# Performance work log

Hardware: AMD Instinct MI355X
Metric: run time of the kernel (lower is better)

## Reference

```python
import jax, jax.numpy as jnp
import numpy as np

B, T = 64, 4096
H, I, F = 256, 7, 5
# MLP pyramid: in=H+F=261 -> 2^8..2^3 -> itera_dim
DIMS = [H + F, 256, 128, 64, 32, 16, 8, I]


def _uniform(key, shape, fan_in):
    s = 1.0 / np.sqrt(fan_in)
    return jax.random.uniform(key, shape, jnp.float32, -s, s)


def setup_inputs() -> dict:
    key = jax.random.key(0)
    ks = jax.random.split(key, 32)
    inp = {"x": jax.random.normal(ks[0], (B, T, I + F), jnp.float32)}
    # RNN params (torch nn.RNN layout: W_ih [H,I], W_hh [H,H])
    inp["W_ih"] = _uniform(ks[1], (H, I), H)
    inp["W_hh"] = _uniform(ks[2], (H, H), H)
    inp["b_ih"] = _uniform(ks[3], (H,), H)
    inp["b_hh"] = _uniform(ks[4], (H,), H)
    # fc_V linears
    for j, (din, dout) in enumerate(zip(DIMS[:-1], DIMS[1:])):
        inp[f"W{j}"] = _uniform(ks[5 + 2 * j], (dout, din), din)
        inp[f"b{j}"] = _uniform(ks[6 + 2 * j], (dout,), din)
    return inp


def reference(x, W_ih, W_hh, b_ih, b_hh,
              W0, b0, W1, b1, W2, b2, W3, b3, W4, b4, W5, b5, W6, b6):
    x_itera = x[..., :I]          # [B,T,I]
    x_fixed = x[..., I:]          # [B,T,F]
    # precompute input projection for the whole sequence (one big GEMM)
    xW = jnp.einsum('bti,hi->bth', x_itera, W_ih) + b_ih + b_hh  # [B,T,H]

    def step(h, xw_t):
        h = jnp.tanh(xw_t + h @ W_hh.T)
        return h, h

    h0 = jnp.zeros((x.shape[0], H), x.dtype)
    h_last, ht = jax.lax.scan(step, h0, jnp.swapaxes(xW, 0, 1))  # ht: [T,B,H]
    ht = jnp.swapaxes(ht, 0, 1)                                  # [B,T,H]

    z = jnp.concatenate([ht, x_fixed], axis=-1)                  # [B,T,H+F]
    for W, b in ((W0, b0), (W1, b1), (W2, b2), (W3, b3), (W4, b4), (W5, b5)):
        z = jax.nn.leaky_relu(z @ W.T + b, 0.01)
    ot = z @ W6.T + b6                                           # [B,T,I]
    return ot, h_last[None]                                      # ht_last: [1,B,H]
```

## Files before the change

### kernel.cpp

```cpp
#include <hip/hip_runtime.h>

#define BB 64
#define TT 4096
#define HH 256
#define NTOK (BB * TT)

typedef _Float16 f16;
typedef _Float16 f16x2 __attribute__((ext_vector_type(2)));
typedef _Float16 f16x8 __attribute__((ext_vector_type(8)));
typedef float f32x4 __attribute__((ext_vector_type(4)));
typedef unsigned int uint;
typedef unsigned short ushort;
typedef uint uint4v __attribute__((ext_vector_type(4)));

__device__ __forceinline__ uint packf16(float a, float b) {
    ushort lo = __builtin_bit_cast(ushort, (f16)a);
    ushort hi = __builtin_bit_cast(ushort, (f16)b);
    return (uint)lo | ((uint)hi << 16);
}

__global__ __launch_bounds__(256) void rnn_wswz_kernel(const float* __restrict__ Whh,
                                                       uint4v* __restrict__ Wsw) {
    int gid = blockIdx.x * 256 + threadIdx.x;
    if (gid >= 8192) return;
    int tid = gid >> 5, fi = gid & 31;
    int mt = fi >> 3, ks = fi & 7;
    int lane = tid & 63, w = tid >> 6;
    int hd = w * 64 + mt * 16 + (lane & 15);
    int kb = ks * 32 + ((lane >> 4) << 3);
    const float* p = Whh + hd * 256 + kb;
    uint4v v;
    v.x = packf16(p[0], p[1]);
    v.y = packf16(p[2], p[3]);
    v.z = packf16(p[4], p[5]);
    v.w = packf16(p[6], p[7]);
    Wsw[gid] = v;
}

__global__ __launch_bounds__(256) void bfrag_prep_kernel(const float* __restrict__ W,
                                                         uint4v* __restrict__ dst,
                                                         int N, int Kreal, int KS, int NT) {
    int gid = blockIdx.x * 256 + threadIdx.x;
    if (gid >= NT * KS * 64) return;
    int lane = gid & 63;
    int t = gid >> 6;
    int ks = t % KS, nt = t / KS;
    int n = nt * 16 + (lane & 15);
    int kb = ks * 32 + (lane >> 4) * 8;
    float f[8];
#pragma unroll
    for (int j = 0; j < 8; ++j) {
        int k = kb + j;
        f[j] = (n < N && k < Kreal) ? W[n * Kreal + k] : 0.f;
    }
    uint4v v;
    v.x = packf16(f[0], f[1]);
    v.y = packf16(f[2], f[3]);
    v.z = packf16(f[4], f[5]);
    v.w = packf16(f[6], f[7]);
    dst[gid] = v;
}

__global__ __launch_bounds__(256) __attribute__((amdgpu_waves_per_eu(1, 1))) void rnn_kernel(
        const float* __restrict__ x, const uint4v* __restrict__ Wsw,
        const float* __restrict__ Wih, const float* __restrict__ bih,
        const float* __restrict__ bhh, f16* __restrict__ ht, float* __restrict__ hlast) {
    const int b = blockIdx.x, tid = threadIdx.x;
    const int lane = tid & 63, w = tid >> 6;
    const int q = lane >> 4, bl = lane & 15;
    const int d = w * 64 + ((bl >> 2) << 4) + (q << 2) + (bl & 3);
    __shared__ __align__(16) f16 hbuf[2][256];
    __shared__ uint4 xs[2][128];

    uint4v wv[32];
    {
        const uint4v* wp = Wsw + (size_t)tid * 32;
#pragma unroll
        for (int i = 0; i < 32; ++i) wv[i] = wp[i];
    }
#pragma unroll
    for (int i = 0; i < 32; ++i) asm volatile("" : "+v"(wv[i]));

    float wih[7];
#pragma unroll
    for (int i = 0; i < 7; ++i) wih[i] = Wih[d * 7 + i];
    const float bias = bih[d] + bhh[d];

    const float* xb = x + (size_t)b * TT * 12;
    uint4 xpre = make_uint4(0, 0, 0, 0);
    if (tid < 128) {
        int row = tid >> 1, u = tid & 1;
        xs[0][row * 2 + u] = *(const uint4*)(xb + row * 12 + u * 4);
        xpre = *(const uint4*)(xb + (64 + row) * 12 + u * 4);
        ((uint*)hbuf[0])[tid] = 0;
    }
    __syncthreads();

    f16* htp = ht + (size_t)b * TT * 256 + d;

    for (int tb = 0; tb < 256; ++tb) {
#pragma unroll
        for (int k = 0; k < 16; ++k) {
            const int t = tb * 16 + k;
            const int cur = k & 1;
            const int tile = (t >> 6) & 1, tstep = t & 63;

            const float4 xa = ((const float4*)xs[tile])[tstep * 2];
            const float4 xc = ((const float4*)xs[tile])[tstep * 2 + 1];
            float xw = fmaf(xa.x, wih[0], bias);
            xw = fmaf(xa.y, wih[1], xw);
            xw = fmaf(xa.z, wih[2], xw);
            xw = fmaf(xa.w, wih[3], xw);
            xw = fmaf(xc.x, wih[4], xw);
            xw = fmaf(xc.y, wih[5], xw);
            xw = fmaf(xc.z, wih[6], xw);

            const uint4v* hq = (const uint4v*)hbuf[cur];
            uint4v hfr[8];
#pragma unroll
            for (int ks = 0; ks < 8; ++ks) hfr[ks] = hq[ks * 4 + q];

            f32x4 acc[4];
#pragma unroll
            for (int mt = 0; mt < 4; ++mt) acc[mt] = (f32x4){0.f, 0.f, 0.f, 0.f};
#pragma unroll
            for (int ks = 0; ks < 8; ++ks) {
                f16x8 hb = __builtin_bit_cast(f16x8, hfr[ks]);
#pragma unroll
                for (int mt = 0; mt < 4; ++mt)
                    acc[mt] = __builtin_amdgcn_mfma_f32_16x16x32_f16(
                        __builtin_bit_cast(f16x8, wv[mt * 8 + ks]), hb, acc[mt], 0, 0, 0);
            }

            float t0[4];
#pragma unroll
            for (int mt = 0; mt < 4; ++mt) {
                float a01 = (bl & 1) ? acc[mt][1] : acc[mt][0];
                float a23 = (bl & 1) ? acc[mt][3] : acc[mt][2];
                t0[mt] = (bl & 2) ? a23 : a01;
            }
            float u0 = (bl & 4) ? t0[1] : t0[0];
            float u1 = (bl & 4) ? t0[3] : t0[2];
            float pre = ((bl & 8) ? u1 : u0) + xw;

            float e = __expf(-2.0f * pre);
            float rr = __builtin_amdgcn_rcpf(1.0f + e);
            float h = fmaf(2.0f, rr, -1.0f);

            f16 hf = (f16)h;
            hbuf[cur ^ 1][d] = hf;
            htp[(size_t)t * 256] = hf;
            if (tb == 255 && k == 15) hlast[b * 256 + d] = h;

            if (tstep == 32 && tid < 128) {
                int row = tid >> 1, u = tid & 1;
                xs[tile ^ 1][row * 2 + u] = xpre;
                int nt = (t & ~63) + 128 + row;
                if (nt > TT - 1) nt = TT - 1;
                xpre = *(const uint4*)(xb + nt * 12 + u * 4);
            }
            asm volatile("s_waitcnt lgkmcnt(0)\n\ts_barrier" ::: "memory");
        }
    }
}

struct MlpB {
    const uint4v* bf[7];
    const float* bias[7];
};

template <int KS, int NT, bool MSPLIT>
__device__ __forceinline__ void mfma_layer(const uint4v* __restrict__ Bf,
                                           const float* __restrict__ bias, int Nreal,
                                           const uint4v* zin, uint4v* zout,
                                           int w, int lane, int m15, int q) {
    constexpr int NW = MSPLIT ? NT : (NT / 4);
    constexpr int MW = MSPLIT ? 1 : 4;
    const int ntb = MSPLIT ? 0 : w * NW;
    const int mtb = MSPLIT ? w : 0;
    f32x4 acc[MW][NW];
#pragma unroll
    for (int i = 0; i < MW; ++i)
#pragma unroll
        for (int j = 0; j < NW; ++j) acc[i][j] = (f32x4){0.f, 0.f, 0.f, 0.f};

#pragma unroll
    for (int ks = 0; ks < KS; ++ks) {
        f16x8 a[MW];
#pragma unroll
        for (int mt = 0; mt < MW; ++mt)
            a[mt] = __builtin_bit_cast(f16x8, zin[((mtb + mt) * 16 + m15) * 37 + ks * 4 + q]);
#pragma unroll
        for (int nt = 0; nt < NW; ++nt) {
            f16x8 b = __builtin_bit_cast(f16x8, Bf[((size_t)(ntb + nt) * KS + ks) * 64 + lane]);
#pragma unroll
            for (int mt = 0; mt < MW; ++mt)
                acc[mt][nt] =
                    __builtin_amdgcn_mfma_f32_16x16x32_f16(a[mt], b, acc[mt][nt], 0, 0, 0);
        }
    }
    f16* zo = (f16*)zout;
#pragma unroll
    for (int nt = 0; nt < NW; ++nt) {
        const int col = (ntb + nt) * 16 + m15;
        const float bv = (col < Nreal) ? bias[col] : 0.f;
#pragma unroll
        for (int mt = 0; mt < MW; ++mt) {
#pragma unroll
            for (int r = 0; r < 4; ++r) {
                float v = acc[mt][nt][r] + bv;
                v = fmaxf(v, 0.01f * v);
                const int row = (mtb + mt) * 16 + q * 4 + r;
                zo[row * 296 + col] = (f16)v;
            }
        }
    }
}

__global__ __launch_bounds__(256) void mlp_kernel(const f16* __restrict__ ht,
                                                  const float* __restrict__ x,
                                                  MlpB P, float* __restrict__ out) {
    __shared__ uint4v z0[64 * 37];
    __shared__ uint4v z1[64 * 37];
    const int tid = threadIdx.x;
    const int w = tid >> 6, lane = tid & 63;
    const int m15 = lane & 15, q = lane >> 4;
    const int tok0 = blockIdx.x * 64;

    for (int i = tid; i < 64 * 32; i += 256) {
        int r = i >> 5, u = i & 31;
        z0[r * 37 + u] = ((const uint4v*)(ht + (size_t)(tok0 + r) * 256))[u];
    }
    for (int i = tid; i < 64 * 5; i += 256) {
        int r = i / 5, u = 32 + (i % 5);
        uint4v v = {0u, 0u, 0u, 0u};
        if (u == 32) {
            const float* xp = x + (size_t)(tok0 + r) * 12 + 7;
            v.x = packf16(xp[0], xp[1]);
            v.y = packf16(xp[2], xp[3]);
            v.z = packf16(xp[4], 0.f);
        }
        z0[r * 37 + u] = v;
    }
    __syncthreads();

    mfma_layer<9, 16, false>(P.bf[0], P.bias[0], 256, z0, z1, w, lane, m15, q);
    __syncthreads();
    mfma_layer<8, 8, false>(P.bf[1], P.bias[1], 128, z1, z0, w, lane, m15, q);
    __syncthreads();
    mfma_layer<4, 4, false>(P.bf[2], P.bias[2], 64, z0, z1, w, lane, m15, q);
    __syncthreads();
    mfma_layer<2, 2, true>(P.bf[3], P.bias[3], 32, z1, z0, w, lane, m15, q);
    __syncthreads();
    mfma_layer<1, 1, true>(P.bf[4], P.bias[4], 16, z0, z1, w, lane, m15, q);
    __syncthreads();
    mfma_layer<1, 1, true>(P.bf[5], P.bias[5], 8, z1, z0, w, lane, m15, q);
    __syncthreads();

    {
        f16x8 a = __builtin_bit_cast(f16x8, z0[(w * 16 + m15) * 37 + q]);
        f16x8 b = __builtin_bit_cast(f16x8, P.bf[6][lane]);
        f32x4 acc = (f32x4){0.f, 0.f, 0.f, 0.f};
        acc = __builtin_amdgcn_mfma_f32_16x16x32_f16(a, b, acc, 0, 0, 0);
        if (m15 < 7) {
            const float bv = P.bias[6][m15];
#pragma unroll
            for (int r = 0; r < 4; ++r)
                out[(size_t)(tok0 + w * 16 + q * 4 + r) * 7 + m15] = acc[r] + bv;
        }
    }
}

extern "C" void kernel_launch(void* const* d_in, const int* in_sizes, int n_in,
                              void* d_out, int out_size, void* d_ws, size_t ws_size,
                              hipStream_t stream) {
    const float* x = (const float*)d_in[0];
    const float* Wih = (const float*)d_in[1];
    const float* Whh = (const float*)d_in[2];
    const float* bih = (const float*)d_in[3];
    const float* bhh = (const float*)d_in[4];
    const float* W[7];
    const float* bb[7];
    for (int j = 0; j < 7; ++j) {
        W[j] = (const float*)d_in[5 + 2 * j];
        bb[j] = (const float*)d_in[6 + 2 * j];
    }
    float* out = (float*)d_out;

    static const int Kd[7] = {261, 256, 128, 64, 32, 16, 8};
    static const int Nd[7] = {256, 128, 64, 32, 16, 8, 7};
    static const int KSd[7] = {9, 8, 4, 2, 1, 1, 1};
    static const int NTd[7] = {16, 8, 4, 2, 1, 1, 1};

    char* ws = (char*)d_ws;
    f16* ht = (f16*)ws;
    size_t off = (size_t)NTOK * HH * 2;
    uint4v* Wsw = (uint4v*)(ws + off);
    off += (size_t)8192 * 16;
    uint4v* bfp[7];
    for (int j = 0; j < 7; ++j) {
        bfp[j] = (uint4v*)(ws + off);
        off += (size_t)NTd[j] * KSd[j] * 64 * 16;
    }

    rnn_wswz_kernel<<<32, 256, 0, stream>>>(Whh, Wsw);
    for (int j = 0; j < 7; ++j) {
        int cnt = NTd[j] * KSd[j] * 64;
        bfrag_prep_kernel<<<(cnt + 255) / 256, 256, 0, stream>>>(W[j], bfp[j], Nd[j], Kd[j],
                                                                 KSd[j], NTd[j]);
    }

    rnn_kernel<<<BB, 256, 0, stream>>>(x, Wsw, Wih, bih, bhh, ht, out + (size_t)NTOK * 7);

    MlpB P;
    for (int j = 0; j < 7; ++j) {
        P.bf[j] = bfp[j];
        P.bias[j] = bb[j];
    }
    mlp_kernel<<<NTOK / 64, 256, 0, stream>>>(ht, x, P, out);
}
```

Before: 2.112 ms.

## Split RNN recurrence across 8 waves with K-split MFMA and batched ht stores

The recurrent kernel now uses 512 threads (8 waves) per batch row. Each wave owns 32 hidden units instead of 64, so it holds half as many W_hh fragments and issues half as many MFMAs per step. The K dimension is split into two independent accumulator chains that are summed afterwards, which shortens the serial MFMA dependency per timestep. Global ht writes are buffered in registers and flushed every 16 steps, and tanh switches to exp2. The aim is to cut per-step latency in the sequential recurrence, at the cost of a wider barrier across 8 waves and some duplicated lanes that are masked off as non-writers.

```diff
diff --git a/kernel.cpp b/kernel.cpp
--- a/kernel.cpp
+++ b/kernel.cpp
@@ -23,10 +23,10 @@
                                                        uint4v* __restrict__ Wsw) {
     int gid = blockIdx.x * 256 + threadIdx.x;
     if (gid >= 8192) return;
-    int tid = gid >> 5, fi = gid & 31;
+    int tid = gid >> 4, fi = gid & 15;
     int mt = fi >> 3, ks = fi & 7;
     int lane = tid & 63, w = tid >> 6;
-    int hd = w * 64 + mt * 16 + (lane & 15);
+    int hd = w * 32 + mt * 16 + (lane & 15);
     int kb = ks * 32 + ((lane >> 4) << 3);
     const float* p = Whh + hd * 256 + kb;
     uint4v v;
@@ -61,25 +61,26 @@
     dst[gid] = v;
 }
 
-__global__ __launch_bounds__(256) __attribute__((amdgpu_waves_per_eu(1, 1))) void rnn_kernel(
+__global__ __launch_bounds__(512) __attribute__((amdgpu_waves_per_eu(2, 2))) void rnn_kernel(
         const float* __restrict__ x, const uint4v* __restrict__ Wsw,
         const float* __restrict__ Wih, const float* __restrict__ bih,
         const float* __restrict__ bhh, f16* __restrict__ ht, float* __restrict__ hlast) {
     const int b = blockIdx.x, tid = threadIdx.x;
     const int lane = tid & 63, w = tid >> 6;
     const int q = lane >> 4, bl = lane & 15;
-    const int d = w * 64 + ((bl >> 2) << 4) + (q << 2) + (bl & 3);
+    const int d = w * 32 + ((bl >> 3) << 4) + (q << 2) + (bl & 3);
+    const bool writer = (bl & 4) == 0;
     __shared__ __align__(16) f16 hbuf[2][256];
     __shared__ uint4 xs[2][128];
 
-    uint4v wv[32];
+    uint4v wv[16];
     {
-        const uint4v* wp = Wsw + (size_t)tid * 32;
-#pragma unroll
-        for (int i = 0; i < 32; ++i) wv[i] = wp[i];
-    }
-#pragma unroll
-    for (int i = 0; i < 32; ++i) asm volatile("" : "+v"(wv[i]));
+        const uint4v* wp = Wsw + (size_t)tid * 16;
+#pragma unroll
+        for (int i = 0; i < 16; ++i) wv[i] = wp[i];
+    }
+#pragma unroll
+    for (int i = 0; i < 16; ++i) asm volatile("" : "+v"(wv[i]));
 
     float wih[7];
 #pragma unroll
@@ -97,6 +98,7 @@
     __syncthreads();
 
     f16* htp = ht + (size_t)b * TT * 256 + d;
+    ushort hst[16];
 
     for (int tb = 0; tb < 256; ++tb) {
 #pragma unroll
@@ -104,6 +106,26 @@
             const int t = tb * 16 + k;
             const int cur = k & 1;
             const int tile = (t >> 6) & 1, tstep = t & 63;
+
+            const uint4v* hq = (const uint4v*)hbuf[cur];
+            uint4v hfr[8];
+#pragma unroll
+            for (int ks = 0; ks < 8; ++ks) hfr[ks] = hq[ks * 4 + q];
+
+            f32x4 a0 = (f32x4){0.f, 0.f, 0.f, 0.f}, a1 = a0, a2 = a0, a3 = a0;
+#pragma unroll
+            for (int kk = 0; kk < 4; ++kk) {
+                f16x8 hlo = __builtin_bit_cast(f16x8, hfr[kk]);
+                f16x8 hhi = __builtin_bit_cast(f16x8, hfr[4 + kk]);
+                a0 = __builtin_amdgcn_mfma_f32_16x16x32_f16(
+                    __builtin_bit_cast(f16x8, wv[kk]), hlo, a0, 0, 0, 0);
+                a1 = __builtin_amdgcn_mfma_f32_16x16x32_f16(
+                    __builtin_bit_cast(f16x8, wv[4 + kk]), hhi, a1, 0, 0, 0);
+                a2 = __builtin_amdgcn_mfma_f32_16x16x32_f16(
+                    __builtin_bit_cast(f16x8, wv[8 + kk]), hlo, a2, 0, 0, 0);
+                a3 = __builtin_amdgcn_mfma_f32_16x16x32_f16(
+                    __builtin_bit_cast(f16x8, wv[12 + kk]), hhi, a3, 0, 0, 0);
+            }
 
             const float4 xa = ((const float4*)xs[tile])[tstep * 2];
             const float4 xc = ((const float4*)xs[tile])[tstep * 2 + 1];
@@ -115,42 +137,25 @@
             xw = fmaf(xc.y, wih[5], xw);
             xw = fmaf(xc.z, wih[6], xw);
 
-            const uint4v* hq = (const uint4v*)hbuf[cur];
-            uint4v hfr[8];
-#pragma unroll
-            for (int ks = 0; ks < 8; ++ks) hfr[ks] = hq[ks * 4 + q];
-
-            f32x4 acc[4];
-#pragma unroll
-            for (int mt = 0; mt < 4; ++mt) acc[mt] = (f32x4){0.f, 0.f, 0.f, 0.f};
-#pragma unroll
-            for (int ks = 0; ks < 8; ++ks) {
-                f16x8 hb = __builtin_bit_cast(f16x8, hfr[ks]);
-#pragma unroll
-                for (int mt = 0; mt < 4; ++mt)
-                    acc[mt] = __builtin_amdgcn_mfma_f32_16x16x32_f16(
-                        __builtin_bit_cast(f16x8, wv[mt * 8 + ks]), hb, acc[mt], 0, 0, 0);
-            }
-
-            float t0[4];
-#pragma unroll
-            for (int mt = 0; mt < 4; ++mt) {
-                float a01 = (bl & 1) ? acc[mt][1] : acc[mt][0];
-                float a23 = (bl & 1) ? acc[mt][3] : acc[mt][2];
-                t0[mt] = (bl & 2) ? a23 : a01;
-            }
-            float u0 = (bl & 4) ? t0[1] : t0[0];
-            float u1 = (bl & 4) ? t0[3] : t0[2];
-            float pre = ((bl & 8) ? u1 : u0) + xw;
-
-            float e = __expf(-2.0f * pre);
+            f32x4 acc0 = a0 + a1;
+            f32x4 acc1 = a2 + a3;
+
+            float s0 = (bl & 8) ? acc1[0] : acc0[0];
+            float s1 = (bl & 8) ? acc1[1] : acc0[1];
+            float s2 = (bl & 8) ? acc1[2] : acc0[2];
+            float s3 = (bl & 8) ? acc1[3] : acc0[3];
+            float p01 = (bl & 1) ? s1 : s0;
+            float p23 = (bl & 1) ? s3 : s2;
+            float pre = ((bl & 2) ? p23 : p01) + xw;
+
+            float e = __builtin_amdgcn_exp2f(-2.885390082f * pre);
             float rr = __builtin_amdgcn_rcpf(1.0f + e);
             float h = fmaf(2.0f, rr, -1.0f);
 
             f16 hf = (f16)h;
-            hbuf[cur ^ 1][d] = hf;
-            htp[(size_t)t * 256] = hf;
-            if (tb == 255 && k == 15) hlast[b * 256 + d] = h;
+            if (writer) hbuf[cur ^ 1][d] = hf;
+            hst[k] = __builtin_bit_cast(ushort, hf);
+            if (tb == 255 && k == 15 && writer) hlast[b * 256 + d] = h;
 
             if (tstep == 32 && tid < 128) {
                 int row = tid >> 1, u = tid & 1;
@@ -160,6 +165,12 @@
                 xpre = *(const uint4*)(xb + nt * 12 + u * 4);
             }
             asm volatile("s_waitcnt lgkmcnt(0)\n\ts_barrier" ::: "memory");
+        }
+        if (writer) {
+            const size_t base = (size_t)(tb * 16) * 256;
+#pragma unroll
+            for (int k = 0; k < 16; ++k)
+                htp[base + (size_t)k * 256] = __builtin_bit_cast(f16, hst[k]);
         }
     }
 }
@@ -310,7 +321,7 @@
                                                                  KSd[j], NTd[j]);
     }
 
-    rnn_kernel<<<BB, 256, 0, stream>>>(x, Wsw, Wih, bih, bhh, ht, out + (size_t)NTOK * 7);
+    rnn_kernel<<<BB, 512, 0, stream>>>(x, Wsw, Wih, bih, bhh, ht, out + (size_t)NTOK * 7);
 
     MlpB P;
     for (int j = 0; j < 7; ++j) {
```

Result: faster. 1.900 ms (-10.0%).

## Pack two batch sequences per RNN block and batch h_t global stores

Applied to the files above, without the earlier changes.

The RNN kernel now runs two independent batch sequences per 512-thread block (32 blocks instead of 64), each group of four waves holding its own copy of the W_hh fragments and its own shared hbuf/xs. The MFMA recurrence is moved ahead of the input projection so the latency-critical matmul starts first, and tanh uses a raw exp2 intrinsic. h_t values are buffered in registers for 16 steps and written to global memory after each block of steps, taking stores out of the per-step critical path. The shared barrier now couples two sequences, and running two waves per EU halves the per-wave register budget, which may cause register pressure or spills.

```diff
diff --git a/kernel.cpp b/kernel.cpp
--- a/kernel.cpp
+++ b/kernel.cpp
@@ -25,8 +25,8 @@
     if (gid >= 8192) return;
     int tid = gid >> 5, fi = gid & 31;
     int mt = fi >> 3, ks = fi & 7;
-    int lane = tid & 63, w = tid >> 6;
-    int hd = w * 64 + mt * 16 + (lane & 15);
+    int lane = tid & 63, wb = tid >> 6;
+    int hd = wb * 64 + mt * 16 + (lane & 15);
     int kb = ks * 32 + ((lane >> 4) << 3);
     const float* p = Whh + hd * 256 + kb;
     uint4v v;
@@ -61,20 +61,23 @@
     dst[gid] = v;
 }
 
-__global__ __launch_bounds__(256) __attribute__((amdgpu_waves_per_eu(1, 1))) void rnn_kernel(
+__global__ __launch_bounds__(512) __attribute__((amdgpu_waves_per_eu(2, 2))) void rnn_kernel(
         const float* __restrict__ x, const uint4v* __restrict__ Wsw,
         const float* __restrict__ Wih, const float* __restrict__ bih,
         const float* __restrict__ bhh, f16* __restrict__ ht, float* __restrict__ hlast) {
-    const int b = blockIdx.x, tid = threadIdx.x;
+    const int tid = threadIdx.x;
     const int lane = tid & 63, w = tid >> 6;
+    const int wb = w & 3, bat = w >> 2;
+    const int b = blockIdx.x * 2 + bat;
+    const int gtid = tid & 255;
     const int q = lane >> 4, bl = lane & 15;
-    const int d = w * 64 + ((bl >> 2) << 4) + (q << 2) + (bl & 3);
-    __shared__ __align__(16) f16 hbuf[2][256];
-    __shared__ uint4 xs[2][128];
+    const int d = wb * 64 + ((bl >> 2) << 4) + (q << 2) + (bl & 3);
+    __shared__ __align__(16) f16 hbuf[2][2][256];
+    __shared__ uint4 xs[2][2][128];
 
     uint4v wv[32];
     {
-        const uint4v* wp = Wsw + (size_t)tid * 32;
+        const uint4v* wp = Wsw + (size_t)(wb * 64 + lane) * 32;
 #pragma unroll
         for (int i = 0; i < 32; ++i) wv[i] = wp[i];
     }
@@ -88,15 +91,16 @@
 
     const float* xb = x + (size_t)b * TT * 12;
     uint4 xpre = make_uint4(0, 0, 0, 0);
-    if (tid < 128) {
-        int row = tid >> 1, u = tid & 1;
-        xs[0][row * 2 + u] = *(const uint4*)(xb + row * 12 + u * 4);
+    if (gtid < 128) {
+        int row = gtid >> 1, u = gtid & 1;
+        xs[bat][0][row * 2 + u] = *(const uint4*)(xb + row * 12 + u * 4);
         xpre = *(const uint4*)(xb + (64 + row) * 12 + u * 4);
-        ((uint*)hbuf[0])[tid] = 0;
+        ((uint*)hbuf[bat][0])[gtid] = 0;
     }
     __syncthreads();
 
     f16* htp = ht + (size_t)b * TT * 256 + d;
+    ushort hst[16];
 
     for (int tb = 0; tb < 256; ++tb) {
 #pragma unroll
@@ -105,8 +109,25 @@
             const int cur = k & 1;
             const int tile = (t >> 6) & 1, tstep = t & 63;
 
-            const float4 xa = ((const float4*)xs[tile])[tstep * 2];
-            const float4 xc = ((const float4*)xs[tile])[tstep * 2 + 1];
+            const uint4v* hq = (const uint4v*)hbuf[bat][cur];
+            uint4v hfr[8];
+#pragma unroll
+            for (int ks = 0; ks < 8; ++ks) hfr[ks] = hq[ks * 4 + q];
+
+            f32x4 acc[4];
+#pragma unroll
+            for (int mt = 0; mt < 4; ++mt) acc[mt] = (f32x4){0.f, 0.f, 0.f, 0.f};
+#pragma unroll
+            for (int ks = 0; ks < 8; ++ks) {
+                f16x8 hb = __builtin_bit_cast(f16x8, hfr[ks]);
+#pragma unroll
+                for (int mt = 0; mt < 4; ++mt)
+                    acc[mt] = __builtin_amdgcn_mfma_f32_16x16x32_f16(
+                        __builtin_bit_cast(f16x8, wv[mt * 8 + ks]), hb, acc[mt], 0, 0, 0);
+            }
+
+            const float4 xa = ((const float4*)xs[bat][tile])[tstep * 2];
+            const float4 xc = ((const float4*)xs[bat][tile])[tstep * 2 + 1];
             float xw = fmaf(xa.x, wih[0], bias);
             xw = fmaf(xa.y, wih[1], xw);
             xw = fmaf(xa.z, wih[2], xw);
@@ -114,23 +135,6 @@
             xw = fmaf(xc.x, wih[4], xw);
             xw = fmaf(xc.y, wih[5], xw);
             xw = fmaf(xc.z, wih[6], xw);
-
-            const uint4v* hq = (const uint4v*)hbuf[cur];
-            uint4v hfr[8];
-#pragma unroll
-            for (int ks = 0; ks < 8; ++ks) hfr[ks] = hq[ks * 4 + q];
-
-            f32x4 acc[4];
-#pragma unroll
-            for (int mt = 0; mt < 4; ++mt) acc[mt] = (f32x4){0.f, 0.f, 0.f, 0.f};
-#pragma unroll
-            for (int ks = 0; ks < 8; ++ks) {
-                f16x8 hb = __builtin_bit_cast(f16x8, hfr[ks]);
-#pragma unroll
-                for (int mt = 0; mt < 4; ++mt)
-                    acc[mt] = __builtin_amdgcn_mfma_f32_16x16x32_f16(
-                        __builtin_bit_cast(f16x8, wv[mt * 8 + ks]), hb, acc[mt], 0, 0, 0);
-            }
 
             float t0[4];
 #pragma unroll
@@ -143,24 +147,28 @@
             float u1 = (bl & 4) ? t0[3] : t0[2];
             float pre = ((bl & 8) ? u1 : u0) + xw;
 
-            float e = __expf(-2.0f * pre);
+            float e = __builtin_amdgcn_exp2f(-2.885390082f * pre);
             float rr = __builtin_amdgcn_rcpf(1.0f + e);
             float h = fmaf(2.0f, rr, -1.0f);
 
             f16 hf = (f16)h;
-            hbuf[cur ^ 1][d] = hf;
-            htp[(size_t)t * 256] = hf;
+            hbuf[bat][cur ^ 1][d] = hf;
+            hst[k] = __builtin_bit_cast(ushort, hf);
             if (tb == 255 && k == 15) hlast[b * 256 + d] = h;
 
-            if (tstep == 32 && tid < 128) {
-                int row = tid >> 1, u = tid & 1;
-                xs[tile ^ 1][row * 2 + u] = xpre;
+            if (tstep == 32 && gtid < 128) {
+                int row = gtid >> 1, u = gtid & 1;
+                xs[bat][tile ^ 1][row * 2 + u] = xpre;
                 int nt = (t & ~63) + 128 + row;
                 if (nt > TT - 1) nt = TT - 1;
                 xpre = *(const uint4*)(xb + nt * 12 + u * 4);
             }
             asm volatile("s_waitcnt lgkmcnt(0)\n\ts_barrier" ::: "memory");
         }
+        const size_t base = (size_t)(tb * 16) * 256;
+#pragma unroll
+        for (int k = 0; k < 16; ++k)
+            htp[base + (size_t)k * 256] = __builtin_bit_cast(f16, hst[k]);
     }
 }
 
@@ -310,7 +318,7 @@
                                                                  KSd[j], NTd[j]);
     }
 
-    rnn_kernel<<<BB, 256, 0, stream>>>(x, Wsw, Wih, bih, bhh, ht, out + (size_t)NTOK * 7);
+    rnn_kernel<<<BB / 2, 512, 0, stream>>>(x, Wsw, Wih, bih, bhh, ht, out + (size_t)NTOK * 7);
 
     MlpB P;
     for (int j = 0; j < 7; ++j) {
```

New measurement: 2.837 ms. 1.34x slower.

## Split RNN recurrence over K across waves with lane-permute h exchange

Applied to the files above, without the earlier changes.

Repartitions the recurrent matvec so each wave handles a 64-wide K slice for all 256 outputs. The hidden state is kept in registers and gathered via ds_bpermute and DPP instead of an LDS h buffer. Partial sums are reduced through a double-buffered LDS array after one barrier per step. The x input is now loaded directly from global memory each step instead of through a prefetched shared tile, which may expose load latency.

```diff
diff --git a/kernel.cpp b/kernel.cpp
--- a/kernel.cpp
+++ b/kernel.cpp
@@ -6,7 +6,6 @@
 #define NTOK (BB * TT)
 
 typedef _Float16 f16;
-typedef _Float16 f16x2 __attribute__((ext_vector_type(2)));
 typedef _Float16 f16x8 __attribute__((ext_vector_type(8)));
 typedef float f32x4 __attribute__((ext_vector_type(4)));
 typedef unsigned int uint;
@@ -19,16 +18,20 @@
     return (uint)lo | ((uint)hi << 16);
 }
 
+__device__ __forceinline__ uint dpp_xor1_u(uint v) {
+    return (uint)__builtin_amdgcn_update_dpp(0, (int)v, 0xB1, 0xF, 0xF, true);
+}
+
 __global__ __launch_bounds__(256) void rnn_wswz_kernel(const float* __restrict__ Whh,
                                                        uint4v* __restrict__ Wsw) {
     int gid = blockIdx.x * 256 + threadIdx.x;
     if (gid >= 8192) return;
     int tid = gid >> 5, fi = gid & 31;
-    int mt = fi >> 3, ks = fi & 7;
+    int mt = fi >> 1, ks = fi & 1;
     int lane = tid & 63, w = tid >> 6;
-    int hd = w * 64 + mt * 16 + (lane & 15);
-    int kb = ks * 32 + ((lane >> 4) << 3);
-    const float* p = Whh + hd * 256 + kb;
+    int row = 16 * mt + (lane & 15);
+    int col = 64 * w + 32 * ks + 8 * (lane >> 4);
+    const float* p = Whh + row * 256 + col;
     uint4v v;
     v.x = packf16(p[0], p[1]);
     v.y = packf16(p[2], p[3]);
@@ -68,9 +71,8 @@
     const int b = blockIdx.x, tid = threadIdx.x;
     const int lane = tid & 63, w = tid >> 6;
     const int q = lane >> 4, bl = lane & 15;
-    const int d = w * 64 + ((bl >> 2) << 4) + (q << 2) + (bl & 3);
-    __shared__ __align__(16) f16 hbuf[2][256];
-    __shared__ uint4 xs[2][128];
+    const int d = 64 * w + lane;
+    __shared__ float pbuf[2][4][256];
 
     uint4v wv[32];
     {
@@ -78,8 +80,6 @@
 #pragma unroll
         for (int i = 0; i < 32; ++i) wv[i] = wp[i];
     }
-#pragma unroll
-    for (int i = 0; i < 32; ++i) asm volatile("" : "+v"(wv[i]));
 
     float wih[7];
 #pragma unroll
@@ -87,81 +87,69 @@
     const float bias = bih[d] + bhh[d];
 
     const float* xb = x + (size_t)b * TT * 12;
-    uint4 xpre = make_uint4(0, 0, 0, 0);
-    if (tid < 128) {
-        int row = tid >> 1, u = tid & 1;
-        xs[0][row * 2 + u] = *(const uint4*)(xb + row * 12 + u * 4);
-        xpre = *(const uint4*)(xb + (64 + row) * 12 + u * 4);
-        ((uint*)hbuf[0])[tid] = 0;
-    }
-    __syncthreads();
-
     f16* htp = ht + (size_t)b * TT * 256 + d;
-
-    for (int tb = 0; tb < 256; ++tb) {
-#pragma unroll
-        for (int k = 0; k < 16; ++k) {
-            const int t = tb * 16 + k;
-            const int cur = k & 1;
-            const int tile = (t >> 6) & 1, tstep = t & 63;
-
-            const float4 xa = ((const float4*)xs[tile])[tstep * 2];
-            const float4 xc = ((const float4*)xs[tile])[tstep * 2 + 1];
-            float xw = fmaf(xa.x, wih[0], bias);
-            xw = fmaf(xa.y, wih[1], xw);
-            xw = fmaf(xa.z, wih[2], xw);
-            xw = fmaf(xa.w, wih[3], xw);
-            xw = fmaf(xc.x, wih[4], xw);
-            xw = fmaf(xc.y, wih[5], xw);
-            xw = fmaf(xc.z, wih[6], xw);
-
-            const uint4v* hq = (const uint4v*)hbuf[cur];
-            uint4v hfr[8];
-#pragma unroll
-            for (int ks = 0; ks < 8; ++ks) hfr[ks] = hq[ks * 4 + q];
-
-            f32x4 acc[4];
-#pragma unroll
-            for (int mt = 0; mt < 4; ++mt) acc[mt] = (f32x4){0.f, 0.f, 0.f, 0.f};
-#pragma unroll
-            for (int ks = 0; ks < 8; ++ks) {
-                f16x8 hb = __builtin_bit_cast(f16x8, hfr[ks]);
-#pragma unroll
-                for (int mt = 0; mt < 4; ++mt)
-                    acc[mt] = __builtin_amdgcn_mfma_f32_16x16x32_f16(
-                        __builtin_bit_cast(f16x8, wv[mt * 8 + ks]), hb, acc[mt], 0, 0, 0);
-            }
-
-            float t0[4];
-#pragma unroll
-            for (int mt = 0; mt < 4; ++mt) {
-                float a01 = (bl & 1) ? acc[mt][1] : acc[mt][0];
-                float a23 = (bl & 1) ? acc[mt][3] : acc[mt][2];
-                t0[mt] = (bl & 2) ? a23 : a01;
-            }
-            float u0 = (bl & 4) ? t0[1] : t0[0];
-            float u1 = (bl & 4) ? t0[3] : t0[2];
-            float pre = ((bl & 8) ? u1 : u0) + xw;
-
-            float e = __expf(-2.0f * pre);
-            float rr = __builtin_amdgcn_rcpf(1.0f + e);
-            float h = fmaf(2.0f, rr, -1.0f);
-
-            f16 hf = (f16)h;
-            hbuf[cur ^ 1][d] = hf;
-            htp[(size_t)t * 256] = hf;
-            if (tb == 255 && k == 15) hlast[b * 256 + d] = h;
-
-            if (tstep == 32 && tid < 128) {
-                int row = tid >> 1, u = tid & 1;
-                xs[tile ^ 1][row * 2 + u] = xpre;
-                int nt = (t & ~63) + 128 + row;
-                if (nt > TT - 1) nt = TT - 1;
-                xpre = *(const uint4*)(xb + nt * 12 + u * 4);
-            }
-            asm volatile("s_waitcnt lgkmcnt(0)\n\ts_barrier" ::: "memory");
-        }
-    }
+    const int bidx = (lane >> 4) << 5;
+
+    uint hpk = 0;
+
+#define RNN_STEP(BUF, T)                                                                   \
+    {                                                                                      \
+        const float* xt = xb + (size_t)(T) * 12;                                           \
+                                    \
+        uint4v bv0, bv1;                                                                   \
+        bv0.x = (uint)__builtin_amdgcn_ds_bpermute(bidx + 0, (int)hpk);                    \
+        bv0.y = (uint)__builtin_amdgcn_ds_bpermute(bidx + 8, (int)hpk);                    \
+        bv0.z = (uint)__builtin_amdgcn_ds_bpermute(bidx + 16, (int)hpk);                   \
+        bv0.w = (uint)__builtin_amdgcn_ds_bpermute(bidx + 24, (int)hpk);                   \
+        bv1.x = (uint)__builtin_amdgcn_ds_bpermute(bidx + 128, (int)hpk);                  \
+        bv1.y = (uint)__builtin_amdgcn_ds_bpermute(bidx + 136, (int)hpk);                  \
+        bv1.z = (uint)__builtin_amdgcn_ds_bpermute(bidx + 144, (int)hpk);                  \
+        bv1.w = (uint)__builtin_amdgcn_ds_bpermute(bidx + 152, (int)hpk);                  \
+        f16x8 hb0 = __builtin_bit_cast(f16x8, bv0);                                        \
+        f16x8 hb1 = __builtin_bit_cast(f16x8, bv1);                                        \
+        f32x4 acc[16];                                                                     \
+        _Pragma("unroll") for (int mt = 0; mt < 16; ++mt) acc[mt] =                        \
+            __builtin_amdgcn_mfma_f32_16x16x32_f16(__builtin_bit_cast(f16x8, wv[2 * mt]),  \
+                                                   hb0, (f32x4){0.f, 0.f, 0.f, 0.f}, 0, 0, 0); \
+        _Pragma("unroll") for (int mt = 0; mt < 16; ++mt) acc[mt] =                        \
+            __builtin_amdgcn_mfma_f32_16x16x32_f16(                                        \
+                __builtin_bit_cast(f16x8, wv[2 * mt + 1]), hb1, acc[mt], 0, 0, 0);         \
+                             \
+        if (bl == 0) {                                                                     \
+            float* pw = &pbuf[BUF][w][q * 4];                                              \
+            _Pragma("unroll") for (int mt = 0; mt < 16; ++mt)                              \
+                *(f32x4*)(pw + mt * 16) = acc[mt];                                         \
+        }                                                                                  \
+                   \
+        float xw = fmaf(xt[0], wih[0], bias);                                              \
+        xw = fmaf(xt[1], wih[1], xw);                                                      \
+        xw = fmaf(xt[2], wih[2], xw);                                                      \
+        xw = fmaf(xt[3], wih[3], xw);                                                      \
+        xw = fmaf(xt[4], wih[4], xw);                                                      \
+        xw = fmaf(xt[5], wih[5], xw);                                                      \
+        xw = fmaf(xt[6], wih[6], xw);                                                      \
+        asm volatile("s_waitcnt lgkmcnt(0)\n\ts_barrier" ::: "memory");                    \
+                  \
+        const float* pr = &pbuf[BUF][0][d];                                                \
+        float pre = ((pr[0] + pr[256]) + (pr[512] + pr[768])) + xw;                        \
+                                          \
+        float e = __builtin_amdgcn_exp2f(-2.885390082f * pre);                             \
+        float rr = __builtin_amdgcn_rcpf(1.0f + e);                                        \
+        float hv = fmaf(2.0f, rr, -1.0f);                                                  \
+        f16 hf = (f16)hv;                                                                  \
+        htp[(size_t)(T) * 256] = hf;                                                       \
+        if ((T) == TT - 1) hlast[b * 256 + d] = hv;                                        \
+                      \
+        uint my = (uint)__builtin_bit_cast(ushort, hf);                                    \
+        uint pt = dpp_xor1_u(my);                                                          \
+        hpk = (lane & 1) ? ((my << 16) | pt) : ((pt << 16) | my);                          \
+    }
+
+    for (int t = 0; t < TT; t += 2) {
+        RNN_STEP(0, t)
+        RNN_STEP(1, t + 1)
+    }
+#undef RNN_STEP
 }
 
 struct MlpB {
```

Result: slower. 3.994 ms (+89.1%).
